# Kernel tuning notes

Hardware: AMD Instinct MI355X
Metric: run time of the kernel (lower is better)

## Reference

```python
import jax, jax.numpy as jnp
import numpy as np

B, N, H, IN, OUT, AXES = 128, 32, 128, 1, 10, 4


def setup_inputs() -> dict:
    key = jax.random.key(0)
    ks = jax.random.split(key, 6)
    s = 0.05
    return {
        "x": jax.random.normal(ks[0], (B, N, N), jnp.float32),
        "Wx": jax.random.normal(ks[1], (AXES, IN, 3 * H), jnp.float32) * s,
        "U1": jax.random.normal(ks[2], (AXES, H, 3 * H), jnp.float32) * s,
        "U2": jax.random.normal(ks[3], (AXES, H, 3 * H), jnp.float32) * s,
        "b": jnp.zeros((AXES, 3 * H), jnp.float32),
        "Wo": jax.random.normal(ks[4], (AXES * H, OUT), jnp.float32) * s,
        "bo": jnp.zeros((OUT,), jnp.float32),
    }


def _mdgru_cell(xj, h_top, h_left, Wx, U1, U2, b):
    # xj: (B, IN); h_top/h_left: (B, H). Two-predecessor GRU cell.
    gx = xj @ Wx + b          # (B, 3H)
    g1 = h_top @ U1           # (B, 3H)
    g2 = h_left @ U2          # (B, 3H)
    xr, xz, xn = jnp.split(gx, 3, axis=-1)
    r1, z1, n1 = jnp.split(g1, 3, axis=-1)
    r2, z2, n2 = jnp.split(g2, 3, axis=-1)
    r = jax.nn.sigmoid(xr + r1 + r2)
    z = jax.nn.sigmoid(xz + z1 + z2)
    n = jnp.tanh(xn + r * (n1 + n2))
    return (1.0 - z) * n + z * 0.5 * (h_top + h_left)


def _scan_dir(img, Wx, U1, U2, b):
    # img: (N_rows, N_cols, B), oriented so scan runs top-left -> bottom-right.
    n_cols, bsz = img.shape[1], img.shape[2]
    h0 = jnp.zeros((bsz, H), img.dtype)

    def row_step(last_row, x_row):  # last_row: (N_cols, B, H); x_row: (N_cols, B)
        def col_step(h_left, inp):
            xj, h_top = inp
            h = _mdgru_cell(xj[:, None], h_top, h_left, Wx, U1, U2, b)
            return h, h
        _, row = jax.lax.scan(col_step, h0, (x_row, last_row))
        return row, row[-1]

    _, finals = jax.lax.scan(row_step, jnp.zeros((n_cols, bsz, H), img.dtype), img)
    return finals[-1]  # (B, H): hidden at the terminal corner


def reference(x, Wx, U1, U2, b, Wo, bo):
    # x: (B, N, N). Four diagonal scan directions via flips.
    flips = [(False, False), (True, False), (False, True), (True, True)]
    hs = []
    for a, (fi, fj) in enumerate(flips):
        xd = x
        if fi:
            xd = jnp.flip(xd, axis=1)
        if fj:
            xd = jnp.flip(xd, axis=2)
        img = jnp.transpose(xd, (1, 2, 0))  # (N_rows, N_cols, B)
        hs.append(_scan_dir(img, Wx[a], U1[a], U2[a], b[a]))
    final_hidden = jnp.concatenate(hs, axis=1)  # (B, 4H)
    return jax.nn.log_softmax(final_hidden @ Wo + bo, axis=1)
```

## Files before the change

kernel.cpp:

```cpp
#include <hip/hip_runtime.h>
#include <type_traits>


#define B_ 128
#define N_ 32
#define H_ 128
#define TH 384
#define KK 256

#define HBF_PLANE 4224
#define HBF_BUF   16896
#define XD_STEP   256

typedef short bf16x8 __attribute__((ext_vector_type(8)));
typedef float f32x4 __attribute__((ext_vector_type(4)));

__device__ inline ushort f2bf(float f) {
    return (ushort)((__float_as_uint(f) + 0x8000u) >> 16);
}
__device__ inline ushort f2bf_rne(float f) {
    unsigned u = __float_as_uint(f);
    return (ushort)((u + 0x7FFFu + ((u >> 16) & 1u)) >> 16);
}

#define NL2E -1.44269504088896f

__global__ void conv_u(const float* __restrict__ U1, const float* __restrict__ U2,
                       ushort* __restrict__ ubf) {
    __shared__ float t[32][33];
    int bx = blockIdx.x;
    int amat = bx / 48, tile = bx % 48;
    int kt = tile / 12, ntl = tile % 12;
    int a = amat >> 1, mat = amat & 1;
    int kk0 = kt * 32, n0 = ntl * 32;
    int tx = threadIdx.x, ty = threadIdx.y;
    const float* U = mat ? U2 : U1;
#pragma unroll
    for (int r = 0; r < 4; r++)
        t[ty + r * 8][tx] = U[(a * H_ + kk0 + ty + r * 8) * TH + n0 + tx];
    __syncthreads();
#pragma unroll
    for (int r = 0; r < 4; r++) {
        int n = n0 + ty + r * 8;
        int kkl = kk0 + tx;
        ubf[(a * TH + n) * KK + mat * H_ + kkl] = f2bf_rne(t[tx][ty + r * 8]);
    }
}

__global__ __launch_bounds__(512, 2) void scan_all(
    const float* __restrict__ x, const float* __restrict__ Wx,
    const float* __restrict__ bvec, const ushort* __restrict__ ubf,
    float* __restrict__ finals) {

    __shared__ __align__(16) char hbf_c[2 * HBF_BUF];
    __shared__ __align__(16) char xd_c[63 * XD_STEP];

    int bx = blockIdx.x;
    int a = bx >> 6, chunk = bx & 63;
    int tid = threadIdx.x;
    int lane = tid & 63, wn = tid >> 6;
    int l16 = lane & 15, lg = lane >> 4;

    for (int idx = tid; idx < (2 * HBF_BUF) / 4; idx += 512) ((unsigned*)hbf_c)[idx] = 0u;
    for (int idx = tid; idx < (63 * XD_STEP) / 4; idx += 512) ((unsigned*)xd_c)[idx] = 0u;
    __syncthreads();

    const float* xg = x + (chunk * 2) * (N_ * N_);
    for (int cell = tid; cell < 1024; cell += 512) {
        int i = cell >> 5, j = cell & 31;
        int ri = (a & 1) ? (31 - i) : i;
        int cj = (a & 2) ? (31 - j) : j;
        float v0 = xg[ri * 32 + cj];
        float v1 = xg[1024 + ri * 32 + cj];
        *(float2*)(xd_c + (i + j) * XD_STEP + i * 8) = make_float2(v0, v1);
    }

    const ushort* ub = ubf + a * (TH * KK);
    bf16x8 Bf[3][8];
#pragma unroll
    for (int p = 0; p < 3; p++) {
        int n = p * H_ + wn * 16 + l16;
#pragma unroll
        for (int ks = 0; ks < 8; ks++) {
            Bf[p][ks] = *(const bf16x8*)(ub + n * KK + ks * 32 + lg * 8);
            asm volatile("" : "+v"(Bf[p][ks]));
        }
    }

    int hh = wn * 16 + l16;
    float wxp[3], bsp[3];
    {
        float wr = Wx[a * TH + hh], br = bvec[a * TH + hh];
        float wz = Wx[a * TH + H_ + hh], bz = bvec[a * TH + H_ + hh];
        float wq = Wx[a * TH + 2 * H_ + hh], bq = bvec[a * TH + 2 * H_ + hh];
        wxp[0] = wr * NL2E; bsp[0] = br * NL2E;
        wxp[1] = wz * NL2E; bsp[1] = bz * NL2E;
        wxp[2] = wq;        bsp[2] = bq;
    }

    int ciA = l16 >> 1, blA = l16 & 1;
    int aT[4], aL[4], wb[4][2][2];
#pragma unroll
    for (int mt = 0; mt < 4; mt++) {
        int st = mt * 8 + ciA;
        aT[mt] = st * 128 + ((blA * 64 + lg * 16) ^ ((st & 7) << 4));
        int sl = st + 1;
        aL[mt] = sl * 128 + ((blA * 64 + lg * 16) ^ ((sl & 7) << 4));
#pragma unroll
        for (int p2 = 0; p2 < 2; p2++) {
            int sw = mt * 8 + lg * 2 + p2 + 1;
#pragma unroll
            for (int bl = 0; bl < 2; bl++)
                wb[mt][p2][bl] = (hh >> 5) * HBF_PLANE + sw * 128 +
                                 ((bl * 64 + (hh & 31) * 2) ^ ((sw & 7) << 4));
        }
    }

    const char* xdp = xd_c + lg * 16;
    __syncthreads();

    float hp[4][2][2];
#pragma unroll
    for (int mt = 0; mt < 4; mt++)
#pragma unroll
        for (int p2 = 0; p2 < 2; p2++)
#pragma unroll
            for (int bl = 0; bl < 2; bl++) hp[mt][p2][bl] = 0.0f;

    int slsrc = (lane - 16) & 63;

    auto step = [&](int d, auto WRC) {
        constexpr int WRB = decltype(WRC)::value;
        constexpr int RDB = WRB ^ 1;
        const char* hbr = hbf_c + RDB * HBF_BUF;
        char* hbw = hbf_c + WRB * HBF_BUF;

        float sh[4][2];
#pragma unroll
        for (int mt = 0; mt < 4; mt++)
#pragma unroll
            for (int bl = 0; bl < 2; bl++)
                sh[mt][bl] = __shfl(hp[mt][1][bl], slsrc, 64);

        bool gm[4];
        f32x4 xv[4];
#pragma unroll
        for (int mt = 0; mt < 4; mt++) {
            gm[mt] = (d >= mt * 8) && (d <= mt * 8 + 38);
            if (gm[mt]) xv[mt] = *(const f32x4*)(xdp + WRB * 256 + mt * 64);
        }

        f32x4 acc[4][3];
        const f32x4 z4 = {0.0f, 0.0f, 0.0f, 0.0f};

        auto do_mfma = [&](int mt) {
            bf16x8 af[8];
#pragma unroll
            for (int ks = 0; ks < 4; ks++) {
                af[ks] = *(const bf16x8*)(hbr + ks * HBF_PLANE + aT[mt]);
                af[ks + 4] = *(const bf16x8*)(hbr + ks * HBF_PLANE + aL[mt]);
            }
#pragma unroll
            for (int ks = 0; ks < 4; ks++)
#pragma unroll
                for (int p = 0; p < 3; p++)
                    acc[mt][p] = __builtin_amdgcn_mfma_f32_16x16x32_bf16(
                        af[ks], Bf[p][ks], (ks == 0) ? z4 : acc[mt][p], 0, 0, 0);
#pragma unroll
            for (int ks = 0; ks < 4; ks++)
#pragma unroll
                for (int p = 0; p < 3; p++)
                    acc[mt][p] = __builtin_amdgcn_mfma_f32_16x16x32_bf16(
                        af[ks + 4], Bf[p][ks + 4], acc[mt][p], 0, 0, 0);
        };

        auto do_epi = [&](int mt) {
            float hv[2][2];
#pragma unroll
            for (int p2 = 0; p2 < 2; p2++)
#pragma unroll
                for (int bl = 0; bl < 2; bl++) {
                    int r = p2 * 2 + bl;
                    float xb = xv[mt][r];
                    float htop = p2 ? hp[mt][0][bl]
                                    : (lg ? sh[mt][bl]
                                          : (mt ? sh[mt - 1][bl] : 0.0f));
                    float hlft = hp[mt][p2][bl];
                    float Gr = acc[mt][0][r];
                    float Gz = acc[mt][1][r];
                    float Gn = acc[mt][2][r];
                    float ar = __builtin_fmaf(Gr, NL2E, __builtin_fmaf(xb, wxp[0], bsp[0]));
                    float rg = __builtin_amdgcn_rcpf(1.0f + __builtin_amdgcn_exp2f(ar));
                    float az = __builtin_fmaf(Gz, NL2E, __builtin_fmaf(xb, wxp[1], bsp[1]));
                    float ez = __builtin_amdgcn_exp2f(az);
                    float vn = __builtin_fmaf(rg, Gn, __builtin_fmaf(xb, wxp[2], bsp[2]));
                    float en = __builtin_amdgcn_exp2f(vn * (2.0f * NL2E));
                    float pz = 1.0f + ez, pn = 1.0f + en;
                    float rp = __builtin_amdgcn_rcpf(pz * pn);
                    float zg = rp * pn;
                    float ng = __builtin_fmaf(2.0f * rp, pz, -1.0f);
                    float hs = htop + hlft;
                    hv[p2][bl] = __builtin_fmaf(-zg, __builtin_fmaf(-0.5f, hs, ng), ng);
                }
#pragma unroll
            for (int p2 = 0; p2 < 2; p2++)
#pragma unroll
                for (int bl = 0; bl < 2; bl++) {
                    *(ushort*)(hbw + wb[mt][p2][bl]) = f2bf(hv[p2][bl]);
                    hp[mt][p2][bl] = hv[p2][bl];
                }
        };

        if (gm[0]) do_mfma(0);
        if (gm[1]) do_mfma(1);
        if (gm[0]) do_epi(0);
        if (gm[2]) do_mfma(2);
        if (gm[1]) do_epi(1);
        if (gm[3]) do_mfma(3);
        if (gm[2]) do_epi(2);
        if (gm[3]) do_epi(3);

        __syncthreads();
    };

    for (int d = 0; d < 62; d += 2) {
        step(d, std::integral_constant<int, 0>{});
        step(d + 1, std::integral_constant<int, 1>{});
        xdp += 512;
    }
    step(62, std::integral_constant<int, 0>{});

    if (lg == 3) {
        finals[(a * B_ + chunk * 2) * H_ + hh] = hp[3][1][0];
        finals[(a * B_ + chunk * 2 + 1) * H_ + hh] = hp[3][1][1];
    }
}

__global__ void classify(const float* __restrict__ fin, const float* __restrict__ Wo,
                         const float* __restrict__ bo, float* __restrict__ out) {
    int b = blockIdx.x;
    int lane = threadIdx.x;
    float acc[10];
#pragma unroll
    for (int o = 0; o < 10; o++) acc[o] = 0.0f;
#pragma unroll
    for (int kkx = 0; kkx < 8; kkx++) {
        int k = kkx * 64 + lane;
        int a = k >> 7, hh = k & 127;
        float fh = fin[(a * B_ + b) * H_ + hh];
#pragma unroll
        for (int o = 0; o < 10; o++) acc[o] += fh * Wo[k * 10 + o];
    }
    float logits[10];
#pragma unroll
    for (int o = 0; o < 10; o++) {
        float v = acc[o];
#pragma unroll
        for (int off = 32; off; off >>= 1) v += __shfl_xor(v, off, 64);
        logits[o] = v + bo[o];
    }
    float m = logits[0];
#pragma unroll
    for (int o = 1; o < 10; o++) m = fmaxf(m, logits[o]);
    float s = 0.0f;
#pragma unroll
    for (int o = 0; o < 10; o++) s += __expf(logits[o] - m);
    float lse = m + __logf(s);
    if (lane == 0) {
#pragma unroll
        for (int o = 0; o < 10; o++) out[b * 10 + o] = logits[o] - lse;
    }
}

extern "C" void kernel_launch(void* const* d_in, const int* in_sizes, int n_in,
                              void* d_out, int out_size, void* d_ws, size_t ws_size,
                              hipStream_t stream) {
    const float* x = (const float*)d_in[0];
    const float* Wx = (const float*)d_in[1];
    const float* U1 = (const float*)d_in[2];
    const float* U2 = (const float*)d_in[3];
    const float* bv = (const float*)d_in[4];
    const float* Wo = (const float*)d_in[5];
    const float* bo = (const float*)d_in[6];
    float* out = (float*)d_out;

    char* ws = (char*)d_ws;
    ushort* ubf = (ushort*)ws;
    float* finals = (float*)(ws + 786432);

    hipLaunchKernelGGL(conv_u, dim3(384), dim3(32, 8), 0, stream, U1, U2, ubf);
    hipLaunchKernelGGL(scan_all, dim3(256), dim3(512), 0, stream, x, Wx, bv, ubf, finals);
    hipLaunchKernelGGL(classify, dim3(128), dim3(64), 0, stream, finals, Wo, bo, out);
}
```

Measured before the change: 147.4 us.

## Restructure wavefront tiles so each MFMA M-row covers one cell per batch plane

Changes the MFMA M-dimension mapping from interleaved (cell, batch) pairs in 4 tiles to separate per-batch planes with 2 tiles of 16 consecutive diagonal cells each. The hidden-state LDS buffers and x staging move to a per-batch layout with an 80-byte row stride in place of the XOR swizzle. The goal is a simpler tile mapping with fewer predicated tile groups. The trade-off is that rows are still wasted at diagonal edges, and the MFMA-then-epilogue interleave across tiles is dropped.

```diff
diff --git a/kernel.cpp b/kernel.cpp
--- a/kernel.cpp
+++ b/kernel.cpp
@@ -8,9 +8,10 @@
 #define TH 384
 #define KK 256
 
-#define HBF_PLANE 4224
-#define HBF_BUF   16896
-#define XD_STEP   256
+#define PLSTR 2640
+#define BUFSTR 10560
+#define PSTRIDE 21120
+#define XDSTR 8064
 
 typedef short bf16x8 __attribute__((ext_vector_type(8)));
 typedef float f32x4 __attribute__((ext_vector_type(4)));
@@ -52,8 +53,8 @@
     const float* __restrict__ bvec, const ushort* __restrict__ ubf,
     float* __restrict__ finals) {
 
-    __shared__ __align__(16) char hbf_c[2 * HBF_BUF];
-    __shared__ __align__(16) char xd_c[63 * XD_STEP];
+    __shared__ __align__(16) char hbf_c[2 * PSTRIDE];
+    __shared__ __align__(16) char xd_c[2 * XDSTR];
 
     int bx = blockIdx.x;
     int a = bx >> 6, chunk = bx & 63;
@@ -61,18 +62,17 @@
     int lane = tid & 63, wn = tid >> 6;
     int l16 = lane & 15, lg = lane >> 4;
 
-    for (int idx = tid; idx < (2 * HBF_BUF) / 4; idx += 512) ((unsigned*)hbf_c)[idx] = 0u;
-    for (int idx = tid; idx < (63 * XD_STEP) / 4; idx += 512) ((unsigned*)xd_c)[idx] = 0u;
+    for (int idx = tid; idx < (2 * PSTRIDE) / 4; idx += 512) ((unsigned*)hbf_c)[idx] = 0u;
+    for (int idx = tid; idx < (2 * XDSTR) / 4; idx += 512) ((unsigned*)xd_c)[idx] = 0u;
     __syncthreads();
 
     const float* xg = x + (chunk * 2) * (N_ * N_);
-    for (int cell = tid; cell < 1024; cell += 512) {
-        int i = cell >> 5, j = cell & 31;
+    for (int cell = tid; cell < 2048; cell += 512) {
+        int P = cell >> 10, c = cell & 1023;
+        int i = c >> 5, j = c & 31;
         int ri = (a & 1) ? (31 - i) : i;
         int cj = (a & 2) ? (31 - j) : j;
-        float v0 = xg[ri * 32 + cj];
-        float v1 = xg[1024 + ri * 32 + cj];
-        *(float2*)(xd_c + (i + j) * XD_STEP + i * 8) = make_float2(v0, v1);
+        *(float*)(xd_c + P * XDSTR + (i + j) * 128 + i * 4) = xg[P * 1024 + ri * 32 + cj];
     }
 
     const ushort* ub = ubf + a * (TH * KK);
@@ -98,141 +98,132 @@
         wxp[2] = wq;        bsp[2] = bq;
     }
 
-    int ciA = l16 >> 1, blA = l16 & 1;
-    int aT[4], aL[4], wb[4][2][2];
-#pragma unroll
-    for (int mt = 0; mt < 4; mt++) {
-        int st = mt * 8 + ciA;
-        aT[mt] = st * 128 + ((blA * 64 + lg * 16) ^ ((st & 7) << 4));
-        int sl = st + 1;
-        aL[mt] = sl * 128 + ((blA * 64 + lg * 16) ^ ((sl & 7) << 4));
-#pragma unroll
-        for (int p2 = 0; p2 < 2; p2++) {
-            int sw = mt * 8 + lg * 2 + p2 + 1;
-#pragma unroll
-            for (int bl = 0; bl < 2; bl++)
-                wb[mt][p2][bl] = (hh >> 5) * HBF_PLANE + sw * 128 +
-                                 ((bl * 64 + (hh & 31) * 2) ^ ((sw & 7) << 4));
-        }
+    int aT[2], wbs[2];
+#pragma unroll
+    for (int mt = 0; mt < 2; mt++) {
+        aT[mt] = (mt * 16 + l16) * 80 + lg * 16;
+        wbs[mt] = (wn >> 1) * PLSTR + (mt * 16 + lg * 4 + 1) * 80 +
+                  ((wn & 1) * 16 + l16) * 2;
     }
 
     const char* xdp = xd_c + lg * 16;
     __syncthreads();
 
-    float hp[4][2][2];
-#pragma unroll
-    for (int mt = 0; mt < 4; mt++)
-#pragma unroll
-        for (int p2 = 0; p2 < 2; p2++)
-#pragma unroll
-            for (int bl = 0; bl < 2; bl++) hp[mt][p2][bl] = 0.0f;
+    float hp[2][2][4];
+#pragma unroll
+    for (int P = 0; P < 2; P++)
+#pragma unroll
+        for (int mt = 0; mt < 2; mt++)
+#pragma unroll
+            for (int r = 0; r < 4; r++) hp[P][mt][r] = 0.0f;
 
     int slsrc = (lane - 16) & 63;
 
-    auto step = [&](int d, auto WRC) {
+    auto step = [&](int d, const char* xp, auto WRC) {
         constexpr int WRB = decltype(WRC)::value;
         constexpr int RDB = WRB ^ 1;
-        const char* hbr = hbf_c + RDB * HBF_BUF;
-        char* hbw = hbf_c + WRB * HBF_BUF;
-
-        float sh[4][2];
-#pragma unroll
-        for (int mt = 0; mt < 4; mt++)
-#pragma unroll
-            for (int bl = 0; bl < 2; bl++)
-                sh[mt][bl] = __shfl(hp[mt][1][bl], slsrc, 64);
-
-        bool gm[4];
-        f32x4 xv[4];
-#pragma unroll
-        for (int mt = 0; mt < 4; mt++) {
-            gm[mt] = (d >= mt * 8) && (d <= mt * 8 + 38);
-            if (gm[mt]) xv[mt] = *(const f32x4*)(xdp + WRB * 256 + mt * 64);
-        }
-
-        f32x4 acc[4][3];
+
+        bool gm0 = (d <= 46);
+        bool gm1 = (d >= 16);
+
+        f32x4 xv[2][2];
+#pragma unroll
+        for (int P = 0; P < 2; P++) {
+            if (gm0) xv[P][0] = *(const f32x4*)(xp + P * XDSTR);
+            if (gm1) xv[P][1] = *(const f32x4*)(xp + P * XDSTR + 64);
+        }
+        float sh[2][2];
+#pragma unroll
+        for (int P = 0; P < 2; P++)
+#pragma unroll
+            for (int mt = 0; mt < 2; mt++)
+                sh[P][mt] = __shfl(hp[P][mt][3], slsrc, 64);
+
+        f32x4 acc[2][2][3];
         const f32x4 z4 = {0.0f, 0.0f, 0.0f, 0.0f};
 
-        auto do_mfma = [&](int mt) {
-            bf16x8 af[8];
-#pragma unroll
-            for (int ks = 0; ks < 4; ks++) {
-                af[ks] = *(const bf16x8*)(hbr + ks * HBF_PLANE + aT[mt]);
-                af[ks + 4] = *(const bf16x8*)(hbr + ks * HBF_PLANE + aL[mt]);
+#pragma unroll
+        for (int P = 0; P < 2; P++) {
+            const char* hbr = hbf_c + P * PSTRIDE + RDB * BUFSTR;
+#pragma unroll
+            for (int mt = 0; mt < 2; mt++) {
+                bool g = mt ? gm1 : gm0;
+                if (g) {
+                    bf16x8 af[8];
+#pragma unroll
+                    for (int ks = 0; ks < 4; ks++) {
+                        af[ks] = *(const bf16x8*)(hbr + ks * PLSTR + aT[mt]);
+                        af[ks + 4] = *(const bf16x8*)(hbr + ks * PLSTR + aT[mt] + 80);
+                    }
+#pragma unroll
+                    for (int ks = 0; ks < 4; ks++)
+#pragma unroll
+                        for (int p = 0; p < 3; p++)
+                            acc[P][mt][p] = __builtin_amdgcn_mfma_f32_16x16x32_bf16(
+                                af[ks], Bf[p][ks], (ks == 0) ? z4 : acc[P][mt][p], 0, 0, 0);
+#pragma unroll
+                    for (int ks = 0; ks < 4; ks++)
+#pragma unroll
+                        for (int p = 0; p < 3; p++)
+                            acc[P][mt][p] = __builtin_amdgcn_mfma_f32_16x16x32_bf16(
+                                af[ks + 4], Bf[p][ks + 4], acc[P][mt][p], 0, 0, 0);
+                }
             }
-#pragma unroll
-            for (int ks = 0; ks < 4; ks++)
-#pragma unroll
-                for (int p = 0; p < 3; p++)
-                    acc[mt][p] = __builtin_amdgcn_mfma_f32_16x16x32_bf16(
-                        af[ks], Bf[p][ks], (ks == 0) ? z4 : acc[mt][p], 0, 0, 0);
-#pragma unroll
-            for (int ks = 0; ks < 4; ks++)
-#pragma unroll
-                for (int p = 0; p < 3; p++)
-                    acc[mt][p] = __builtin_amdgcn_mfma_f32_16x16x32_bf16(
-                        af[ks + 4], Bf[p][ks + 4], acc[mt][p], 0, 0, 0);
-        };
-
-        auto do_epi = [&](int mt) {
-            float hv[2][2];
-#pragma unroll
-            for (int p2 = 0; p2 < 2; p2++)
-#pragma unroll
-                for (int bl = 0; bl < 2; bl++) {
-                    int r = p2 * 2 + bl;
-                    float xb = xv[mt][r];
-                    float htop = p2 ? hp[mt][0][bl]
-                                    : (lg ? sh[mt][bl]
-                                          : (mt ? sh[mt - 1][bl] : 0.0f));
-                    float hlft = hp[mt][p2][bl];
-                    float Gr = acc[mt][0][r];
-                    float Gz = acc[mt][1][r];
-                    float Gn = acc[mt][2][r];
-                    float ar = __builtin_fmaf(Gr, NL2E, __builtin_fmaf(xb, wxp[0], bsp[0]));
-                    float rg = __builtin_amdgcn_rcpf(1.0f + __builtin_amdgcn_exp2f(ar));
-                    float az = __builtin_fmaf(Gz, NL2E, __builtin_fmaf(xb, wxp[1], bsp[1]));
-                    float ez = __builtin_amdgcn_exp2f(az);
-                    float vn = __builtin_fmaf(rg, Gn, __builtin_fmaf(xb, wxp[2], bsp[2]));
-                    float en = __builtin_amdgcn_exp2f(vn * (2.0f * NL2E));
-                    float pz = 1.0f + ez, pn = 1.0f + en;
-                    float rp = __builtin_amdgcn_rcpf(pz * pn);
-                    float zg = rp * pn;
-                    float ng = __builtin_fmaf(2.0f * rp, pz, -1.0f);
-                    float hs = htop + hlft;
-                    hv[p2][bl] = __builtin_fmaf(-zg, __builtin_fmaf(-0.5f, hs, ng), ng);
+        }
+
+#pragma unroll
+        for (int P = 0; P < 2; P++) {
+            char* hbw = hbf_c + P * PSTRIDE + WRB * BUFSTR;
+#pragma unroll
+            for (int mt = 0; mt < 2; mt++) {
+                bool g = mt ? gm1 : gm0;
+                if (g) {
+                    float hv[4];
+#pragma unroll
+                    for (int r = 0; r < 4; r++) {
+                        float xb = xv[P][mt][r];
+                        float htop = r ? hp[P][mt][r - 1]
+                                       : (mt ? (lg ? sh[P][1] : sh[P][0])
+                                             : (lg ? sh[P][0] : 0.0f));
+                        float hlft = hp[P][mt][r];
+                        float Gr = acc[P][mt][0][r];
+                        float Gz = acc[P][mt][1][r];
+                        float Gn = acc[P][mt][2][r];
+                        float ar = __builtin_fmaf(Gr, NL2E, __builtin_fmaf(xb, wxp[0], bsp[0]));
+                        float rg = __builtin_amdgcn_rcpf(1.0f + __builtin_amdgcn_exp2f(ar));
+                        float az = __builtin_fmaf(Gz, NL2E, __builtin_fmaf(xb, wxp[1], bsp[1]));
+                        float ez = __builtin_amdgcn_exp2f(az);
+                        float vn = __builtin_fmaf(rg, Gn, __builtin_fmaf(xb, wxp[2], bsp[2]));
+                        float en = __builtin_amdgcn_exp2f(vn * (2.0f * NL2E));
+                        float pz = 1.0f + ez, pn = 1.0f + en;
+                        float rp = __builtin_amdgcn_rcpf(pz * pn);
+                        float zg = rp * pn;
+                        float ng = __builtin_fmaf(2.0f * rp, pz, -1.0f);
+                        float hs = htop + hlft;
+                        hv[r] = __builtin_fmaf(-zg, __builtin_fmaf(-0.5f, hs, ng), ng);
+                    }
+#pragma unroll
+                    for (int r = 0; r < 4; r++) {
+                        *(ushort*)(hbw + wbs[mt] + r * 80) = f2bf(hv[r]);
+                        hp[P][mt][r] = hv[r];
+                    }
                 }
-#pragma unroll
-            for (int p2 = 0; p2 < 2; p2++)
-#pragma unroll
-                for (int bl = 0; bl < 2; bl++) {
-                    *(ushort*)(hbw + wb[mt][p2][bl]) = f2bf(hv[p2][bl]);
-                    hp[mt][p2][bl] = hv[p2][bl];
-                }
-        };
-
-        if (gm[0]) do_mfma(0);
-        if (gm[1]) do_mfma(1);
-        if (gm[0]) do_epi(0);
-        if (gm[2]) do_mfma(2);
-        if (gm[1]) do_epi(1);
-        if (gm[3]) do_mfma(3);
-        if (gm[2]) do_epi(2);
-        if (gm[3]) do_epi(3);
-
+            }
+        }
         __syncthreads();
     };
 
+    const char* xp = xdp;
     for (int d = 0; d < 62; d += 2) {
-        step(d, std::integral_constant<int, 0>{});
-        step(d + 1, std::integral_constant<int, 1>{});
-        xdp += 512;
-    }
-    step(62, std::integral_constant<int, 0>{});
+        step(d, xp, std::integral_constant<int, 0>{});
+        step(d + 1, xp + 128, std::integral_constant<int, 1>{});
+        xp += 256;
+    }
+    step(62, xp, std::integral_constant<int, 0>{});
 
     if (lg == 3) {
-        finals[(a * B_ + chunk * 2) * H_ + hh] = hp[3][1][0];
-        finals[(a * B_ + chunk * 2 + 1) * H_ + hh] = hp[3][1][1];
+        finals[(a * B_ + chunk * 2) * H_ + hh] = hp[0][1][3];
+        finals[(a * B_ + chunk * 2 + 1) * H_ + hh] = hp[1][1][3];
     }
 }
 
```

New measurement: 173.3 us. 1.18x slower.

## Switch recurrent GEMM from bf16 to fp8 MFMA with compact LDS layout

Applied to the files above, without the earlier changes.

Converts the recurrent weight matrices and the hidden-state LDS buffer from bf16 to fp8 and uses the 16x16x32 fp8 MFMA in place of the bf16 one. The LDS hidden-state layout is rebuilt with a smaller padded stride and no XOR swizzle, which halves the bytes per A-fragment load and per weight register. The intent is to cut LDS traffic and register pressure on the serial scan's critical path. The cost is much lower precision in the 32-row-by-32-column recurrence, which may push errors past tolerance, and the unswizzled layout and byte-wise stores may cause bank conflicts.

```diff
diff --git a/kernel.cpp b/kernel.cpp
--- a/kernel.cpp
+++ b/kernel.cpp
@@ -8,25 +8,20 @@
 #define TH 384
 #define KK 256
 
-#define HBF_PLANE 4224
-#define HBF_BUF   16896
-#define XD_STEP   256
-
-typedef short bf16x8 __attribute__((ext_vector_type(8)));
+#define PLSTR 2640
+#define BUFSTR 10560
+#define XD_STEP 256
+
 typedef float f32x4 __attribute__((ext_vector_type(4)));
 
-__device__ inline ushort f2bf(float f) {
-    return (ushort)((__float_as_uint(f) + 0x8000u) >> 16);
-}
-__device__ inline ushort f2bf_rne(float f) {
-    unsigned u = __float_as_uint(f);
-    return (ushort)((u + 0x7FFFu + ((u >> 16) & 1u)) >> 16);
+__device__ inline unsigned cvt2fp8(float a, float b) {
+    return (unsigned)__builtin_amdgcn_cvt_pk_fp8_f32(a, b, 0, false);
 }
 
 #define NL2E -1.44269504088896f
 
 __global__ void conv_u(const float* __restrict__ U1, const float* __restrict__ U2,
-                       ushort* __restrict__ ubf) {
+                       char* __restrict__ ub8) {
     __shared__ float t[32][33];
     int bx = blockIdx.x;
     int amat = bx / 48, tile = bx % 48;
@@ -43,16 +38,17 @@
     for (int r = 0; r < 4; r++) {
         int n = n0 + ty + r * 8;
         int kkl = kk0 + tx;
-        ubf[(a * TH + n) * KK + mat * H_ + kkl] = f2bf_rne(t[tx][ty + r * 8]);
+        unsigned pk = cvt2fp8(t[tx][ty + r * 8], 0.0f);
+        ub8[(a * TH + n) * KK + mat * H_ + kkl] = (char)(pk & 0xFF);
     }
 }
 
 __global__ __launch_bounds__(512, 2) void scan_all(
     const float* __restrict__ x, const float* __restrict__ Wx,
-    const float* __restrict__ bvec, const ushort* __restrict__ ubf,
+    const float* __restrict__ bvec, const char* __restrict__ ubf8,
     float* __restrict__ finals) {
 
-    __shared__ __align__(16) char hbf_c[2 * HBF_BUF];
+    __shared__ __align__(16) char hbf_c[2 * BUFSTR];
     __shared__ __align__(16) char xd_c[63 * XD_STEP];
 
     int bx = blockIdx.x;
@@ -61,7 +57,7 @@
     int lane = tid & 63, wn = tid >> 6;
     int l16 = lane & 15, lg = lane >> 4;
 
-    for (int idx = tid; idx < (2 * HBF_BUF) / 4; idx += 512) ((unsigned*)hbf_c)[idx] = 0u;
+    for (int idx = tid; idx < (2 * BUFSTR) / 4; idx += 512) ((unsigned*)hbf_c)[idx] = 0u;
     for (int idx = tid; idx < (63 * XD_STEP) / 4; idx += 512) ((unsigned*)xd_c)[idx] = 0u;
     __syncthreads();
 
@@ -75,14 +71,14 @@
         *(float2*)(xd_c + (i + j) * XD_STEP + i * 8) = make_float2(v0, v1);
     }
 
-    const ushort* ub = ubf + a * (TH * KK);
-    bf16x8 Bf[3][8];
+    const char* ub = ubf8 + a * (TH * KK);
+    long Bf[3][8];
 #pragma unroll
     for (int p = 0; p < 3; p++) {
         int n = p * H_ + wn * 16 + l16;
 #pragma unroll
         for (int ks = 0; ks < 8; ks++) {
-            Bf[p][ks] = *(const bf16x8*)(ub + n * KK + ks * 32 + lg * 8);
+            Bf[p][ks] = *(const long*)(ub + n * KK + ks * 32 + lg * 8);
             asm volatile("" : "+v"(Bf[p][ks]));
         }
     }
@@ -98,22 +94,12 @@
         wxp[2] = wq;        bsp[2] = bq;
     }
 
-    int ciA = l16 >> 1, blA = l16 & 1;
-    int aT[4], aL[4], wb[4][2][2];
+    int aT[4], wbs[4];
 #pragma unroll
     for (int mt = 0; mt < 4; mt++) {
-        int st = mt * 8 + ciA;
-        aT[mt] = st * 128 + ((blA * 64 + lg * 16) ^ ((st & 7) << 4));
-        int sl = st + 1;
-        aL[mt] = sl * 128 + ((blA * 64 + lg * 16) ^ ((sl & 7) << 4));
-#pragma unroll
-        for (int p2 = 0; p2 < 2; p2++) {
-            int sw = mt * 8 + lg * 2 + p2 + 1;
-#pragma unroll
-            for (int bl = 0; bl < 2; bl++)
-                wb[mt][p2][bl] = (hh >> 5) * HBF_PLANE + sw * 128 +
-                                 ((bl * 64 + (hh & 31) * 2) ^ ((sw & 7) << 4));
-        }
+        aT[mt] = (mt * 16 + l16) * 40 + lg * 8;
+        wbs[mt] = (wn >> 1) * PLSTR + ((mt * 8 + lg * 2 + 1) * 2) * 40 +
+                  (wn & 1) * 16 + l16;
     }
 
     const char* xdp = xd_c + lg * 16;
@@ -132,8 +118,8 @@
     auto step = [&](int d, auto WRC) {
         constexpr int WRB = decltype(WRC)::value;
         constexpr int RDB = WRB ^ 1;
-        const char* hbr = hbf_c + RDB * HBF_BUF;
-        char* hbw = hbf_c + WRB * HBF_BUF;
+        const char* hbr = hbf_c + RDB * BUFSTR;
+        char* hbw = hbf_c + WRB * BUFSTR;
 
         float sh[4][2];
 #pragma unroll
@@ -154,23 +140,23 @@
         const f32x4 z4 = {0.0f, 0.0f, 0.0f, 0.0f};
 
         auto do_mfma = [&](int mt) {
-            bf16x8 af[8];
+            long af[8];
 #pragma unroll
             for (int ks = 0; ks < 4; ks++) {
-                af[ks] = *(const bf16x8*)(hbr + ks * HBF_PLANE + aT[mt]);
-                af[ks + 4] = *(const bf16x8*)(hbr + ks * HBF_PLANE + aL[mt]);
+                af[ks] = *(const long*)(hbr + ks * PLSTR + aT[mt]);
+                af[ks + 4] = *(const long*)(hbr + ks * PLSTR + aT[mt] + 80);
             }
 #pragma unroll
             for (int ks = 0; ks < 4; ks++)
 #pragma unroll
                 for (int p = 0; p < 3; p++)
-                    acc[mt][p] = __builtin_amdgcn_mfma_f32_16x16x32_bf16(
+                    acc[mt][p] = __builtin_amdgcn_mfma_f32_16x16x32_fp8_fp8(
                         af[ks], Bf[p][ks], (ks == 0) ? z4 : acc[mt][p], 0, 0, 0);
 #pragma unroll
             for (int ks = 0; ks < 4; ks++)
 #pragma unroll
                 for (int p = 0; p < 3; p++)
-                    acc[mt][p] = __builtin_amdgcn_mfma_f32_16x16x32_bf16(
+                    acc[mt][p] = __builtin_amdgcn_mfma_f32_16x16x32_fp8_fp8(
                         af[ks + 4], Bf[p][ks + 4], acc[mt][p], 0, 0, 0);
         };
 
@@ -203,12 +189,14 @@
                     hv[p2][bl] = __builtin_fmaf(-zg, __builtin_fmaf(-0.5f, hs, ng), ng);
                 }
 #pragma unroll
-            for (int p2 = 0; p2 < 2; p2++)
-#pragma unroll
-                for (int bl = 0; bl < 2; bl++) {
-                    *(ushort*)(hbw + wb[mt][p2][bl]) = f2bf(hv[p2][bl]);
-                    hp[mt][p2][bl] = hv[p2][bl];
-                }
+            for (int p2 = 0; p2 < 2; p2++) {
+                unsigned pk = cvt2fp8(hv[p2][0], hv[p2][1]);
+                char* wp = hbw + wbs[mt] + p2 * 80;
+                wp[0] = (char)(pk & 0xFF);
+                wp[40] = (char)((pk >> 8) & 0xFF);
+#pragma unroll
+                for (int bl = 0; bl < 2; bl++) hp[mt][p2][bl] = hv[p2][bl];
+            }
         };
 
         if (gm[0]) do_mfma(0);
@@ -285,10 +273,10 @@
     float* out = (float*)d_out;
 
     char* ws = (char*)d_ws;
-    ushort* ubf = (ushort*)ws;
-    float* finals = (float*)(ws + 786432);
-
-    hipLaunchKernelGGL(conv_u, dim3(384), dim3(32, 8), 0, stream, U1, U2, ubf);
-    hipLaunchKernelGGL(scan_all, dim3(256), dim3(512), 0, stream, x, Wx, bv, ubf, finals);
+    char* ub8 = ws;
+    float* finals = (float*)(ws + 393216);
+
+    hipLaunchKernelGGL(conv_u, dim3(384), dim3(32, 8), 0, stream, U1, U2, ub8);
+    hipLaunchKernelGGL(scan_all, dim3(256), dim3(512), 0, stream, x, Wx, bv, ub8, finals);
     hipLaunchKernelGGL(classify, dim3(128), dim3(64), 0, stream, finals, Wo, bo, out);
 }
```

Measured after the change: 145.7 us. No clear change (-1.2%).
